# Performance work log

Hardware: AMD Instinct MI355X
Metric: run time of the kernel (lower is better)

Reference implementation:

```python
import jax, jax.numpy as jnp
import numpy as np

N_EMBD = 768
N_HEAD = 12
HEAD_DIM = N_EMBD // N_HEAD


def setup_inputs() -> dict:
    key = jax.random.key(0)
    k0, k1, k2, k3, k4 = jax.random.split(key, 5)
    B, T, C = 2, 4096, N_EMBD
    x = jax.random.normal(k0, (B, T, C), dtype=jnp.float32)
    # c_attn: Linear(C, 3C); c_proj: Linear(C, C). torch Linear: y = x @ W.T + b
    s = 1.0 / np.sqrt(C)
    W_attn = jax.random.uniform(k1, (3 * C, C), dtype=jnp.float32, minval=-s, maxval=s)
    b_attn = jax.random.uniform(k2, (3 * C,), dtype=jnp.float32, minval=-s, maxval=s)
    W_proj = jax.random.uniform(k3, (C, C), dtype=jnp.float32, minval=-s, maxval=s)
    b_proj = jax.random.uniform(k4, (C,), dtype=jnp.float32, minval=-s, maxval=s)
    return {"x": x, "W_attn": W_attn, "b_attn": b_attn, "W_proj": W_proj, "b_proj": b_proj}


def reference(x, W_attn, b_attn, W_proj, b_proj):
    B, T, C = x.shape
    H, D = N_HEAD, HEAD_DIM
    qkv = x @ W_attn.T + b_attn                      # [B,T,3C]
    q, k, v = jnp.split(qkv, 3, axis=-1)
    # [B,T,C] -> [B,H,T,D]
    q = q.reshape(B, T, H, D).transpose(0, 2, 1, 3)
    k = k.reshape(B, T, H, D).transpose(0, 2, 1, 3)
    v = v.reshape(B, T, H, D).transpose(0, 2, 1, 3)
    scale = 1.0 / jnp.sqrt(jnp.asarray(D, dtype=x.dtype))
    att = jnp.einsum('bhqd,bhkd->bhqk', q, k) * scale  # [B,H,T,T]
    att = jax.nn.softmax(att, axis=-1)
    y = jnp.einsum('bhqk,bhkd->bhqd', att, v)          # [B,H,T,D]
    y = y.transpose(0, 2, 1, 3).reshape(B, T, C)
    return y @ W_proj.T + b_proj
```

## Files before the change

kernel.cpp:

```cpp
#include <hip/hip_runtime.h>
#include <stdint.h>
#include <stddef.h>

typedef __bf16 bf16_t;
typedef bf16_t bf16x4 __attribute__((ext_vector_type(4)));
typedef bf16_t bf16x8 __attribute__((ext_vector_type(8)));
typedef float  f32x4  __attribute__((ext_vector_type(4)));
typedef _Float16 f16_t;
typedef f16_t f16x2 __attribute__((ext_vector_type(2)));
typedef f16_t f16x4 __attribute__((ext_vector_type(4)));
typedef f16_t f16x8 __attribute__((ext_vector_type(8)));
typedef __fp16 fp16x2_raw __attribute__((ext_vector_type(2)));

__device__ __forceinline__ f16x2 pkrtz(float a, float b) {
    fp16x2_raw r = __builtin_amdgcn_cvt_pkrtz(a, b);
    union { fp16x2_raw r; f16x2 h; } u;
    u.r = r;
    return u.h;
}

#define MFMA_BF16_K32(a, b, c) __builtin_amdgcn_mfma_f32_16x16x32_bf16(a, b, c, 0, 0, 0)
#define MFMA_F16_K32(a, b, c)  __builtin_amdgcn_mfma_f32_16x16x32_f16(a, b, c, 0, 0, 0)

__device__ __forceinline__ void gload_lds16(const void* g, void* l) {
    __builtin_amdgcn_global_load_lds(
        (const __attribute__((address_space(1))) void*)g,
        (__attribute__((address_space(3))) void*)l,
        16, 0, 0);
}

#define NX 1572864
#define NWA 442368
#define NWP 147456
__global__ void cvt_all(const float* __restrict__ x, const float* __restrict__ Wa,
                        const float* __restrict__ Wp, bf16_t* __restrict__ xb,
                        bf16_t* __restrict__ Wab, bf16_t* __restrict__ Wpb) {
    int i = blockIdx.x * blockDim.x + threadIdx.x;
    const float4* src; bf16_t* dst; int j;
    if (i < NX)            { src = (const float4*)x;  dst = xb;  j = i; }
    else if (i < NX + NWA) { src = (const float4*)Wa; dst = Wab; j = i - NX; }
    else                   { src = (const float4*)Wp; dst = Wpb; j = i - NX - NWA; }
    float4 f = src[j];
    bf16x4 o = { (bf16_t)f.x, (bf16_t)f.y, (bf16_t)f.z, (bf16_t)f.w };
    ((bf16x4*)dst)[j] = o;
}

template <int KDIM>
__device__ __forceinline__ void gemm_mainloop(
    const bf16_t* __restrict__ A, const bf16_t* __restrict__ Bt,
    bf16_t* As, bf16_t* Bs, int m0, int n0, int wave, int lane, f32x4 acc[4][4])
{
    const int quad = lane >> 4, l15 = lane & 15;
    const int wm = ((wave >> 1) << 6), wn = ((wave & 1) << 6);

    const int srow = (wave << 4) + (lane >> 2);
    const int sw   = (((lane & 3) ^ ((srow >> 1) & 3)) << 3);
    const bf16_t* gA = A  + (size_t)(m0 + srow) * KDIM + sw;
    const bf16_t* gB = Bt + (size_t)(n0 + srow) * KDIM + sw;
    bf16_t* lA0 = As + wave * 512;
    bf16_t* lA1 = As + 2048 + wave * 512;
    bf16_t* lB0 = Bs + wave * 512;
    bf16_t* lB1 = Bs + 2048 + wave * 512;

    const int xorv = ((quad ^ ((l15 >> 1) & 3)) << 3);

    for (int k0 = 0; k0 < KDIM; k0 += 32) {
        __syncthreads();
        gload_lds16(gA + k0,                       lA0);
        gload_lds16(gA + (size_t)64 * KDIM + k0,   lA1);
        gload_lds16(gB + k0,                       lB0);
        gload_lds16(gB + (size_t)64 * KDIM + k0,   lB1);
        __syncthreads();

        bf16x8 af[4], bfr[4];
#pragma unroll
        for (int t = 0; t < 4; t++) {
            af[t]  = *(const bf16x8*)(As + (wm + t * 16 + l15) * 32 + xorv);
            bfr[t] = *(const bf16x8*)(Bs + (wn + t * 16 + l15) * 32 + xorv);
        }
#pragma unroll
        for (int mt = 0; mt < 4; mt++)
#pragma unroll
            for (int nt = 0; nt < 4; nt++)
                acc[mt][nt] = MFMA_BF16_K32(af[mt], bfr[nt], acc[mt][nt]);
    }
}

__global__ __launch_bounds__(256) void gemm_qkv(
    const bf16_t* __restrict__ A,
    const bf16_t* __restrict__ Bt,
    const float* __restrict__ bias,
    bf16_t* __restrict__ qo, bf16_t* __restrict__ ko, f16_t* __restrict__ vo)
{
    __shared__ bf16_t As[128 * 32];
    __shared__ bf16_t Bs[128 * 32];
    const int tid = threadIdx.x, wave = tid >> 6, lane = tid & 63;
    const int quad = lane >> 4, l15 = lane & 15;
    const int m0 = blockIdx.y * 128, n0 = blockIdx.x * 128;
    f32x4 acc[4][4] = {};
    gemm_mainloop<768>(A, Bt, As, Bs, m0, n0, wave, lane, acc);

    const int wm = ((wave >> 1) << 6), wn = ((wave & 1) << 6);
#pragma unroll
    for (int nt = 0; nt < 4; nt++) {
        const int cc = n0 + wn + nt * 16 + l15;
        const float bia = bias[cc];
        const int which = cc / 768;
        const int rem = cc - which * 768;
        const int h = rem >> 6, d = rem & 63;
        if (which < 2) {
            bf16_t* dst = (which == 0) ? qo : ko;
#pragma unroll
            for (int mt = 0; mt < 4; mt++) {
#pragma unroll
                for (int r = 0; r < 4; r++) {
                    const int row = m0 + wm + mt * 16 + quad * 4 + r;
                    const int b = row >> 12, t = row & 4095;
                    dst[((size_t)(b * 12 + h) * 4096 + t) * 64 + d] =
                        (bf16_t)(acc[mt][nt][r] + bia);
                }
            }
        } else {
#pragma unroll
            for (int mt = 0; mt < 4; mt++) {
                const int row0 = m0 + wm + mt * 16 + quad * 4;
                const int b = row0 >> 12, t0 = row0 & 4095;
                f16x4 ov = { (f16_t)(acc[mt][nt][0] + bia),
                             (f16_t)(acc[mt][nt][1] + bia),
                             (f16_t)(acc[mt][nt][2] + bia),
                             (f16_t)(acc[mt][nt][3] + bia) };
                *(f16x4*)(vo + ((size_t)(b * 12 + h) * 64 + d) * 4096 + t0) = ov;
            }
        }
    }
}

__global__ __launch_bounds__(256) void gemm_proj(
    const bf16_t* __restrict__ A,
    const bf16_t* __restrict__ Bt,
    const float* __restrict__ bias,
    float* __restrict__ out)
{
    __shared__ bf16_t As[128 * 32];
    __shared__ bf16_t Bs[128 * 32];
    const int tid = threadIdx.x, wave = tid >> 6, lane = tid & 63;
    const int quad = lane >> 4, l15 = lane & 15;
    const int m0 = blockIdx.y * 128, n0 = blockIdx.x * 128;
    f32x4 acc[4][4] = {};
    gemm_mainloop<768>(A, Bt, As, Bs, m0, n0, wave, lane, acc);

    const int wm = ((wave >> 1) << 6), wn = ((wave & 1) << 6);
#pragma unroll
    for (int nt = 0; nt < 4; nt++) {
        const int cc = n0 + wn + nt * 16 + l15;
        const float bia = bias[cc];
#pragma unroll
        for (int mt = 0; mt < 4; mt++) {
#pragma unroll
            for (int r = 0; r < 4; r++) {
                const int row = m0 + wm + mt * 16 + quad * 4 + r;
                out[(size_t)row * 768 + cc] = acc[mt][nt][r] + bia;
            }
        }
    }
}

#define QSCALE 0.1803368801f
__global__ __launch_bounds__(256, 2) void attn_fwd(
    const bf16_t* __restrict__ qg, const bf16_t* __restrict__ kg,
    const f16_t* __restrict__ vtg, bf16_t* __restrict__ y)
{
    __shared__ __align__(16) char smem[65536];
    bf16_t* Ks0 = (bf16_t*)(smem);
    bf16_t* Ks1 = (bf16_t*)(smem + 8192);
    bf16_t* Ks2 = (bf16_t*)(smem + 16384);
    bf16_t* Ks3 = (bf16_t*)(smem + 24576);
    f16_t*  Vt0 = (f16_t*)(smem + 32768);
    f16_t*  Vt1 = (f16_t*)(smem + 40960);
    f16_t*  Vt2 = (f16_t*)(smem + 49152);
    f16_t*  Vt3 = (f16_t*)(smem + 57344);
    float*  RedA = (float*)(smem);
    float*  RedB = (float*)(smem + 17408);
    float*  Psr  = (float*)(smem + 34816);
    float*  PsT  = (float*)(smem + 35840);

    const int tid = threadIdx.x, wave = tid >> 6, lane = tid & 63;
    const int quad = lane >> 4, l15 = lane & 15;

    const int blk = blockIdx.x;
    const int xcd = blk & 7;
    const int idx = blk >> 3;
    const int hl  = idx % 3;
    const int qt  = idx / 3;
    const int bh  = xcd * 3 + hl;
    const int b = bh / 12, h = bh - b * 12;
    const size_t base = (size_t)bh * 4096 * 64;

    bf16x8 qf[4][2];
#pragma unroll
    for (int qc = 0; qc < 4; qc++) {
        const int qrow = qt * 64 + qc * 16 + l15;
        qf[qc][0] = *(const bf16x8*)(qg + base + (size_t)qrow * 64 + quad * 8);
        qf[qc][1] = *(const bf16x8*)(qg + base + (size_t)qrow * 64 + 32 + quad * 8);
#pragma unroll
        for (int j = 0; j < 8; j++) {
            qf[qc][0][j] = (bf16_t)((float)qf[qc][0][j] * QSCALE);
            qf[qc][1][j] = (bf16_t)((float)qf[qc][1][j] * QSCALE);
        }
    }

    f32x4 O[4][4] = {};
    float psum[4] = {};
    const f16x2 one2 = { (f16_t)1.0f, (f16_t)1.0f };

    const int srow8 = tid >> 3;
    const int sc8   = (tid & 7) ^ (srow8 & 7);
    const int l8 = l15 & 7;
    const int w16 = wave << 4;
    const int ksoff = (quad ^ l8) << 3;
    const int vslot = ((wave << 1) | (quad >> 1)) ^ l8;
    const int q0off = (quad & 1) * 8;

    auto stage = [&](const bf16_t* kp_, const f16_t* vp_, bf16_t* Kd, f16_t* Vd) {
#pragma unroll
        for (int i = 0; i < 2; i++) {
            gload_lds16(kp_ + (i * 32 + srow8) * 64 + sc8 * 8,           Kd + (i * 256 + tid) * 8);
            gload_lds16(vp_ + (size_t)(i * 32 + srow8) * 4096 + sc8 * 8, Vd + (i * 256 + tid) * 8);
        }
    };

    auto compute_pair = [&](const bf16_t* ksA, const f16_t* vsA,
                            const bf16_t* ksB, const f16_t* vsB) {
        const bf16_t* krA = ksA + (w16 + l15) * 64;
        const bf16_t* krB = ksB + (w16 + l15) * 64;
        bf16x8 kfA0 = *(const bf16x8*)(krA + ksoff);
        bf16x8 kfA1 = *(const bf16x8*)(krA + (ksoff ^ 32));
        bf16x8 kfB0 = *(const bf16x8*)(krB + ksoff);
        bf16x8 kfB1 = *(const bf16x8*)(krB + (ksoff ^ 32));
        f32x4 scA[4], scB[4];
        __builtin_amdgcn_s_setprio(1);
#pragma unroll
        for (int qc = 0; qc < 4; qc++) {
            f32x4 s = {};
            s = MFMA_BF16_K32(kfA0, qf[qc][0], s);
            s = MFMA_BF16_K32(kfA1, qf[qc][1], s);
            scA[qc] = s;
        }
#pragma unroll
        for (int qc = 0; qc < 4; qc++) {
            f32x4 s = {};
            s = MFMA_BF16_K32(kfB0, qf[qc][0], s);
            s = MFMA_BF16_K32(kfB1, qf[qc][1], s);
            scB[qc] = s;
        }
        __builtin_amdgcn_s_setprio(0);
        f16x8 pf8[4];
#pragma unroll
        for (int qc = 0; qc < 4; qc++) {
            float a0 = __builtin_amdgcn_exp2f(scA[qc][0]);
            float a1 = __builtin_amdgcn_exp2f(scA[qc][1]);
            float a2 = __builtin_amdgcn_exp2f(scA[qc][2]);
            float a3 = __builtin_amdgcn_exp2f(scA[qc][3]);
            float b0 = __builtin_amdgcn_exp2f(scB[qc][0]);
            float b1 = __builtin_amdgcn_exp2f(scB[qc][1]);
            float b2 = __builtin_amdgcn_exp2f(scB[qc][2]);
            float b3 = __builtin_amdgcn_exp2f(scB[qc][3]);
            f16x2 loA = pkrtz(a0, a1);
            f16x2 hiA = pkrtz(a2, a3);
            f16x2 loB = pkrtz(b0, b1);
            f16x2 hiB = pkrtz(b2, b3);
            psum[qc] = __builtin_amdgcn_fdot2(loA, one2, psum[qc], false);
            psum[qc] = __builtin_amdgcn_fdot2(hiA, one2, psum[qc], false);
            psum[qc] = __builtin_amdgcn_fdot2(loB, one2, psum[qc], false);
            psum[qc] = __builtin_amdgcn_fdot2(hiB, one2, psum[qc], false);
            union { f16x8 v; f16x2 h[4]; } u;
            u.h[0] = loA; u.h[1] = hiA; u.h[2] = loB; u.h[3] = hiB;
            pf8[qc] = u.v;
        }
        __builtin_amdgcn_s_setprio(1);
#pragma unroll
        for (int dt = 0; dt < 4; dt++) {
            const char* vrA = (const char*)(vsA + (dt * 16 + l15) * 64);
            const char* vrB = (const char*)(vsB + (dt * 16 + l15) * 64);
            f16x4 vA = *(const f16x4*)(vrA + vslot * 16 + q0off);
            f16x4 vB = *(const f16x4*)(vrB + vslot * 16 + q0off);
            union { f16x8 v; f16x4 h[2]; } uv;
            uv.h[0] = vA; uv.h[1] = vB;
#pragma unroll
            for (int qc = 0; qc < 4; qc++)
                O[dt][qc] = MFMA_F16_K32(uv.v, pf8[qc], O[dt][qc]);
        }
        __builtin_amdgcn_s_setprio(0);
    };

    const bf16_t* kp = kg + base;
    const f16_t*  vp = vtg + base;
    stage(kp, vp, Ks0, Vt0);
    stage(kp + 4096, vp + 64, Ks1, Vt1);
    kp += 8192; vp += 128;
    for (int pt = 0; pt < 32; pt += 2) {
        __syncthreads();
        stage(kp, vp, Ks2, Vt2);
        stage(kp + 4096, vp + 64, Ks3, Vt3);
        kp += 8192; vp += 128;
        compute_pair(Ks0, Vt0, Ks1, Vt1);
        __syncthreads();
        if (pt + 2 < 32) {
            stage(kp, vp, Ks0, Vt0);
            stage(kp + 4096, vp + 64, Ks1, Vt1);
            kp += 8192; vp += 128;
        }
        compute_pair(Ks2, Vt2, Ks3, Vt3);
    }

#pragma unroll
    for (int qc = 0; qc < 4; qc++) {
        psum[qc] += __shfl_xor(psum[qc], 16, 64);
        psum[qc] += __shfl_xor(psum[qc], 32, 64);
    }
    __syncthreads();
    if (wave == 2) {
#pragma unroll
        for (int dt = 0; dt < 4; dt++)
#pragma unroll
            for (int qc = 0; qc < 4; qc++)
                *(f32x4*)(RedA + (qc * 16 + l15) * 68 + dt * 16 + quad * 4) = O[dt][qc];
    } else if (wave == 3) {
#pragma unroll
        for (int dt = 0; dt < 4; dt++)
#pragma unroll
            for (int qc = 0; qc < 4; qc++)
                *(f32x4*)(RedB + (qc * 16 + l15) * 68 + dt * 16 + quad * 4) = O[dt][qc];
    }
    if (quad == 0) {
#pragma unroll
        for (int qc = 0; qc < 4; qc++) Psr[wave * 64 + qc * 16 + l15] = psum[qc];
    }
    __syncthreads();
    if (wave == 0) {
#pragma unroll
        for (int dt = 0; dt < 4; dt++)
#pragma unroll
            for (int qc = 0; qc < 4; qc++)
                O[dt][qc] += *(const f32x4*)(RedA + (qc * 16 + l15) * 68 + dt * 16 + quad * 4);
    } else if (wave == 1) {
#pragma unroll
        for (int dt = 0; dt < 4; dt++)
#pragma unroll
            for (int qc = 0; qc < 4; qc++)
                O[dt][qc] += *(const f32x4*)(RedB + (qc * 16 + l15) * 68 + dt * 16 + quad * 4);
    }
    __syncthreads();
    if (wave == 1) {
#pragma unroll
        for (int dt = 0; dt < 4; dt++)
#pragma unroll
            for (int qc = 0; qc < 4; qc++)
                *(f32x4*)(RedA + (qc * 16 + l15) * 68 + dt * 16 + quad * 4) = O[dt][qc];
    } else if (wave == 3) {
        PsT[lane] = Psr[lane] + Psr[64 + lane] + Psr[128 + lane] + Psr[192 + lane];
    }
    __syncthreads();
    if (wave == 0) {
#pragma unroll
        for (int qc = 0; qc < 4; qc++) {
            const float rcp = 1.0f / PsT[qc * 16 + l15];
            const int t = qt * 64 + qc * 16 + l15;
            bf16_t* yr = y + ((size_t)b * 4096 + t) * 768 + h * 64 + quad * 4;
#pragma unroll
            for (int dt = 0; dt < 4; dt++) {
                f32x4 o4 = O[dt][qc] +
                    *(const f32x4*)(RedA + (qc * 16 + l15) * 68 + dt * 16 + quad * 4);
                bf16x4 ov = { (bf16_t)(o4[0] * rcp), (bf16_t)(o4[1] * rcp),
                              (bf16_t)(o4[2] * rcp), (bf16_t)(o4[3] * rcp) };
                *(bf16x4*)(yr + dt * 16) = ov;
            }
        }
    }
}

extern "C" void kernel_launch(void* const* d_in, const int* in_sizes, int n_in,
                              void* d_out, int out_size, void* d_ws, size_t ws_size,
                              hipStream_t stream) {
    const float* x  = (const float*)d_in[0];
    const float* Wa = (const float*)d_in[1];
    const float* ba = (const float*)d_in[2];
    const float* Wp = (const float*)d_in[3];
    const float* bp = (const float*)d_in[4];
    float* out = (float*)d_out;

    char* ws = (char*)d_ws;
    bf16_t* xb  = (bf16_t*)(ws);
    bf16_t* Wab = (bf16_t*)(ws + 12582912);
    bf16_t* Wpb = (bf16_t*)(ws + 16121856);
    bf16_t* qb  = (bf16_t*)(ws + 17301504);
    bf16_t* kb  = (bf16_t*)(ws + 29884416);
    f16_t*  vtb = (f16_t*)(ws + 42467328);
    bf16_t* yb  = (bf16_t*)(ws + 55050240);

    cvt_all<<<8448, 256, 0, stream>>>(x, Wa, Wp, xb, Wab, Wpb);
    gemm_qkv <<<dim3(18, 64), 256, 0, stream>>>(xb, Wab, ba, qb, kb, vtb);
    attn_fwd <<<1536, 256, 0, stream>>>(qb, kb, vtb, yb);
    gemm_proj<<<dim3( 6, 64), 256, 0, stream>>>(yb, Wpb, bp, out);
}
```

Measured before the change: 273.6 us.

## Load V operand directly from global into registers, shrink LDS for 3 blocks/CU

V^T tiles are no longer staged through shared memory. Each lane now reads its f16x4 V fragments straight from global memory into registers just before the PV MFMAs. This cuts LDS usage from 64KB to 36KB and raises launch bounds to 3 blocks per CU for more occupancy. The cost is more register pressure, and the V loads are issued right before use, so their global latency may not be hidden.

```diff
diff --git a/kernel.cpp b/kernel.cpp
--- a/kernel.cpp
+++ b/kernel.cpp
@@ -166,19 +166,15 @@
 }
 
 #define QSCALE 0.1803368801f
-__global__ __launch_bounds__(256, 2) void attn_fwd(
+__global__ __launch_bounds__(256, 3) void attn_fwd(
     const bf16_t* __restrict__ qg, const bf16_t* __restrict__ kg,
     const f16_t* __restrict__ vtg, bf16_t* __restrict__ y)
 {
-    __shared__ __align__(16) char smem[65536];
+    __shared__ __align__(16) char smem[36864];
     bf16_t* Ks0 = (bf16_t*)(smem);
     bf16_t* Ks1 = (bf16_t*)(smem + 8192);
     bf16_t* Ks2 = (bf16_t*)(smem + 16384);
     bf16_t* Ks3 = (bf16_t*)(smem + 24576);
-    f16_t*  Vt0 = (f16_t*)(smem + 32768);
-    f16_t*  Vt1 = (f16_t*)(smem + 40960);
-    f16_t*  Vt2 = (f16_t*)(smem + 49152);
-    f16_t*  Vt3 = (f16_t*)(smem + 57344);
     float*  RedA = (float*)(smem);
     float*  RedB = (float*)(smem + 17408);
     float*  Psr  = (float*)(smem + 34816);
@@ -218,19 +214,22 @@
     const int l8 = l15 & 7;
     const int w16 = wave << 4;
     const int ksoff = (quad ^ l8) << 3;
-    const int vslot = ((wave << 1) | (quad >> 1)) ^ l8;
-    const int q0off = (quad & 1) * 8;
-
-    auto stage = [&](const bf16_t* kp_, const f16_t* vp_, bf16_t* Kd, f16_t* Vd) {
-#pragma unroll
-        for (int i = 0; i < 2; i++) {
-            gload_lds16(kp_ + (i * 32 + srow8) * 64 + sc8 * 8,           Kd + (i * 256 + tid) * 8);
-            gload_lds16(vp_ + (size_t)(i * 32 + srow8) * 4096 + sc8 * 8, Vd + (i * 256 + tid) * 8);
-        }
+
+    auto stage = [&](const bf16_t* kp_, bf16_t* Kd) {
+#pragma unroll
+        for (int i = 0; i < 2; i++)
+            gload_lds16(kp_ + (i * 32 + srow8) * 64 + sc8 * 8, Kd + (i * 256 + tid) * 8);
     };
 
-    auto compute_pair = [&](const bf16_t* ksA, const f16_t* vsA,
-                            const bf16_t* ksB, const f16_t* vsB) {
+    auto vload = [&](const f16_t* vb_, f16x4 vv[4][2]) {
+#pragma unroll
+        for (int dt = 0; dt < 4; dt++) {
+            vv[dt][0] = *(const f16x4*)(vb_ + (size_t)dt * 65536);
+            vv[dt][1] = *(const f16x4*)(vb_ + (size_t)dt * 65536 + 64);
+        }
+    };
+
+    auto compute_pair = [&](const bf16_t* ksA, const bf16_t* ksB, const f16x4 vv[4][2]) {
         const bf16_t* krA = ksA + (w16 + l15) * 64;
         const bf16_t* krB = ksB + (w16 + l15) * 64;
         bf16x8 kfA0 = *(const bf16x8*)(krA + ksoff);
@@ -280,12 +279,8 @@
         __builtin_amdgcn_s_setprio(1);
 #pragma unroll
         for (int dt = 0; dt < 4; dt++) {
-            const char* vrA = (const char*)(vsA + (dt * 16 + l15) * 64);
-            const char* vrB = (const char*)(vsB + (dt * 16 + l15) * 64);
-            f16x4 vA = *(const f16x4*)(vrA + vslot * 16 + q0off);
-            f16x4 vB = *(const f16x4*)(vrB + vslot * 16 + q0off);
             union { f16x8 v; f16x4 h[2]; } uv;
-            uv.h[0] = vA; uv.h[1] = vB;
+            uv.h[0] = vv[dt][0]; uv.h[1] = vv[dt][1];
 #pragma unroll
             for (int qc = 0; qc < 4; qc++)
                 O[dt][qc] = MFMA_F16_K32(uv.v, pf8[qc], O[dt][qc]);
@@ -294,23 +289,19 @@
     };
 
     const bf16_t* kp = kg + base;
-    const f16_t*  vp = vtg + base;
-    stage(kp, vp, Ks0, Vt0);
-    stage(kp + 4096, vp + 64, Ks1, Vt1);
-    kp += 8192; vp += 128;
-    for (int pt = 0; pt < 32; pt += 2) {
+    const f16_t*  vb = vtg + base + (size_t)l15 * 4096 + w16 + quad * 4;
+    stage(kp, Ks0); stage(kp + 4096, Ks1); kp += 8192;
+    f16x4 v0[4][2], v1[4][2];
+    for (int p = 0; p < 32; p += 2) {
         __syncthreads();
-        stage(kp, vp, Ks2, Vt2);
-        stage(kp + 4096, vp + 64, Ks3, Vt3);
-        kp += 8192; vp += 128;
-        compute_pair(Ks0, Vt0, Ks1, Vt1);
+        vload(vb, v0);
+        stage(kp, Ks2); stage(kp + 4096, Ks3); kp += 8192;
+        compute_pair(Ks0, Ks1, v0);
         __syncthreads();
-        if (pt + 2 < 32) {
-            stage(kp, vp, Ks0, Vt0);
-            stage(kp + 4096, vp + 64, Ks1, Vt1);
-            kp += 8192; vp += 128;
-        }
-        compute_pair(Ks2, Vt2, Ks3, Vt3);
+        vload(vb + 128, v1);
+        if (p + 2 < 32) { stage(kp, Ks0); stage(kp + 4096, Ks1); kp += 8192; }
+        compute_pair(Ks2, Ks3, v1);
+        vb += 256;
     }
 
 #pragma unroll
```

Result: slower. 474.6 us (+73.4%).
